# Kernel optimization log

Hardware: AMD Instinct MI355X
Metric: run time of the kernel (lower is better)

The kernel has to match this reference:

```python
import jax, jax.numpy as jnp
import numpy as np
from jax import lax

SEQ_SIZE = 4096
V = 4                               # vocab size
B = 256                             # batch
FILTER_SIZES = [4, 5, 6, 7, 8]
H = 10                              # lstm hidden
I = (len(FILTER_SIZES) + 1) * V     # lstm input size = 24


def setup_inputs() -> dict:
    key = jax.random.key(0)
    ks = jax.random.split(key, 9)
    inp = {"x": jax.random.normal(ks[0], (B, 1, V * SEQ_SIZE), dtype=jnp.float32)}
    for fs in FILTER_SIZES:
        # matches nn.init.constant_(conv.weight, 0.01)
        inp[f"w{fs}"] = jnp.full((1, 1, fs), 0.01, dtype=jnp.float32)
    s = 1.0 / float(np.sqrt(H))
    shapes = {"Wih": (4 * H, I), "Whh": (4 * H, H), "bih": (4 * H,), "bhh": (4 * H,)}
    k = 1
    for d in ("f", "r"):
        for nm, sh in shapes.items():
            inp[f"{nm}_{d}"] = jax.random.uniform(ks[k], sh, jnp.float32, -s, s)
            k += 1
    return inp


def _branch(x, w, fs):
    # x: (B,1,V*S); conv1d stride=V, VALID, no bias -> (B,1,L)
    conv = lax.conv_general_dilated(x, w, window_strides=(V,), padding="VALID",
                                    dimension_numbers=("NCH", "OIH", "NCH"))
    # winner_takes_all: (x + max_over_len)^2
    m = jnp.max(conv, axis=2, keepdims=True)
    v = ((conv + m) ** 2)[:, 0, :]                                  # (B,L)
    Bsz, L = v.shape
    # shape_convolutions2 == scatter-add of v[b,i] into out[b, V*i + j], j<fs
    idx = (V * jnp.arange(L)[:, None] + jnp.arange(fs)[None, :]).reshape(-1)
    contrib = jnp.broadcast_to(v[:, :, None], (Bsz, L, fs)).reshape(Bsz, -1)
    out = jnp.zeros((Bsz, V * SEQ_SIZE), v.dtype).at[:, idx].add(contrib)
    return out.reshape(Bsz, SEQ_SIZE, V)


def _lstm_dir(xs, Wih, Whh, bih, bhh, reverse):
    # xs: (S,B,I) -> hidden states (S,B,H), aligned with input positions
    Bsz = xs.shape[1]
    h0 = jnp.zeros((Bsz, H), xs.dtype)
    c0 = jnp.zeros((Bsz, H), xs.dtype)
    b = bih + bhh

    def step(carry, xt):
        h, c = carry
        g = xt @ Wih.T + h @ Whh.T + b          # (B,4H), torch gate order i,f,g,o
        i, f, gg, o = jnp.split(g, 4, axis=1)
        c = jax.nn.sigmoid(f) * c + jax.nn.sigmoid(i) * jnp.tanh(gg)
        h = jax.nn.sigmoid(o) * jnp.tanh(c)
        return (h, c), h

    _, hs = lax.scan(step, (h0, c0), xs, reverse=reverse)
    return hs


def _forward(x, ws, Wih_f, Whh_f, bih_f, bhh_f, Wih_r, Whh_r, bih_r, bhh_r):
    Bsz = x.shape[0]
    branches = [_branch(x, w, fs) for w, fs in zip(ws, FILTER_SIZES)]
    inp_r = x.reshape(Bsz, SEQ_SIZE, V)
    l_lstmin = jnp.concatenate(branches + [inp_r], axis=2)   # (B,S,24)
    xs = jnp.swapaxes(l_lstmin, 0, 1)                        # (S,B,24)
    hf = _lstm_dir(xs, Wih_f, Whh_f, bih_f, bhh_f, False)
    hr = _lstm_dir(xs, Wih_r, Whh_r, bih_r, bhh_r, True)
    h_sum = jnp.sum(hf, axis=2) + jnp.sum(hr, axis=2)        # (S,B)
    h_sum = h_sum.T                                          # (B,S)
    # l_in * repeated h_sum, reshaped and summed over vocab == inp_r * h_sum
    l_profile = jnp.sum(inp_r * h_sum[:, :, None], axis=2)   # (B,S)
    return jax.nn.sigmoid(jnp.sum(l_profile, axis=1, keepdims=True))  # (B,1)


def reference(x, w4, w5, w6, w7, w8, Wih_f, Whh_f, bih_f, bhh_f, Wih_r, Whh_r, bih_r, bhh_r):
    return _forward(x, [w4, w5, w6, w7, w8],
                    Wih_f, Whh_f, bih_f, bhh_f, Wih_r, Whh_r, bih_r, bhh_r)
```

## Files before the change

### kernel.cpp

```cpp
#include <hip/hip_runtime.h>

#define SEQ 4096
#define NBATCH 256

typedef float v2f __attribute__((ext_vector_type(2)));

__device__ __forceinline__ float sqf(float v) { return v * v; }
__device__ __forceinline__ float fexp2(float v) { return __builtin_amdgcn_exp2f(v); }
__device__ __forceinline__ float frcp(float v)  { return __builtin_amdgcn_rcpf(v); }

#define L2E 1.4426950408889634f

__device__ __forceinline__ unsigned fkey(float f) {
    const int b = __float_as_int(f);
    return (unsigned)(b ^ ((b >> 31) | 0x80000000));
}
__device__ __forceinline__ float fival(unsigned k) {
    const int b = (k & 0x80000000u) ? (int)(k ^ 0x80000000u) : (int)(~k);
    return __int_as_float(b);
}

__global__ void wprep_kernel(
    const float* __restrict__ Wih_f, const float* __restrict__ bih_f,
    const float* __restrict__ bhh_f,
    const float* __restrict__ Wih_r, const float* __restrict__ bih_r,
    const float* __restrict__ bhh_r,
    float* __restrict__ Wp, unsigned* __restrict__ MMu)
{
    const int t = threadIdx.x;
    for (int i = t; i < NBATCH * 5; i += 256) MMu[i] = 0u;
    if (t >= 80) return;
    const int d = t / 40, r = t % 40;
    const float* __restrict__ W  = (d ? Wih_r : Wih_f) + r * 24;
    const float* __restrict__ bi = d ? bih_r : bih_f;
    const float* __restrict__ bh = d ? bhh_r : bhh_f;
    const float sc = (r >= 20 && r < 30) ? (-2.f * L2E) : (-L2E);
    float o[13];
    o[0]  = W[0] + W[1] + W[2] + W[3];
    o[1]  = W[4] + W[5] + W[6] + W[7];
    o[2]  = W[4];
    o[3]  = W[8] + W[9] + W[10] + W[11];
    o[4]  = W[8] + W[9];
    o[5]  = W[12] + W[13] + W[14] + W[15];
    o[6]  = W[12] + W[13] + W[14];
    o[7]  = W[16] + W[17] + W[18] + W[19];
    o[8]  = W[20]; o[9] = W[21]; o[10] = W[22]; o[11] = W[23];
    o[12] = bi[r] + bh[r];
    float* __restrict__ out = Wp + (d * 40 + r) * 16;
#pragma unroll
    for (int k = 0; k < 13; ++k) out[k] = o[k] * sc;
    out[13] = 0.f; out[14] = 0.f; out[15] = 0.f;
}

__global__ __launch_bounds__(256) void max_kernel(
    const float* __restrict__ x,
    const float* __restrict__ w4p, const float* __restrict__ w5p,
    const float* __restrict__ w6p, const float* __restrict__ w7p,
    const float* __restrict__ w8p,
    unsigned* __restrict__ MMu)
{
    const int b    = blockIdx.x >> 2;
    const int quar = blockIdx.x & 3;
    const int tid  = threadIdx.x;
    const float* __restrict__ xr = x + (size_t)b * (4 * SEQ);

    float W4[4], W5[5], W6[6], W7[7], W8[8];
#pragma unroll
    for (int k = 0; k < 4; ++k) W4[k] = w4p[k];
#pragma unroll
    for (int k = 0; k < 5; ++k) W5[k] = w5p[k];
#pragma unroll
    for (int k = 0; k < 6; ++k) W6[k] = w6p[k];
#pragma unroll
    for (int k = 0; k < 7; ++k) W7[k] = w7p[k];
#pragma unroll
    for (int k = 0; k < 8; ++k) W8[k] = w8p[k];

    float m4 = -3.4e38f, m5 = -3.4e38f, m6 = -3.4e38f, m7 = -3.4e38f, m8 = -3.4e38f;
    for (int i = quar * (SEQ / 4) + tid; i < (quar + 1) * (SEQ / 4); i += 256) {
        const float4 t0 = *reinterpret_cast<const float4*>(xr + 4 * i);
        const float xa0 = t0.x, xa1 = t0.y, xa2 = t0.z, xa3 = t0.w;
        const float c4 = xa0 * W4[0] + xa1 * W4[1] + xa2 * W4[2] + xa3 * W4[3];
        m4 = fmaxf(m4, c4);
        if (i < SEQ - 1) {
            const float4 t1 = *reinterpret_cast<const float4*>(xr + 4 * i + 4);
            const float xa4 = t1.x, xa5 = t1.y, xa6 = t1.z, xa7 = t1.w;
            const float c5 = xa0*W5[0]+xa1*W5[1]+xa2*W5[2]+xa3*W5[3]+xa4*W5[4];
            const float c6 = xa0*W6[0]+xa1*W6[1]+xa2*W6[2]+xa3*W6[3]+xa4*W6[4]+xa5*W6[5];
            const float c7 = xa0*W7[0]+xa1*W7[1]+xa2*W7[2]+xa3*W7[3]+xa4*W7[4]+xa5*W7[5]+xa6*W7[6];
            const float c8 = xa0*W8[0]+xa1*W8[1]+xa2*W8[2]+xa3*W8[3]+xa4*W8[4]+xa5*W8[5]+xa6*W8[6]+xa7*W8[7];
            m5 = fmaxf(m5, c5); m6 = fmaxf(m6, c6);
            m7 = fmaxf(m7, c7); m8 = fmaxf(m8, c8);
        }
    }
#pragma unroll
    for (int off = 32; off; off >>= 1) {
        m4 = fmaxf(m4, __shfl_down(m4, off));
        m5 = fmaxf(m5, __shfl_down(m5, off));
        m6 = fmaxf(m6, __shfl_down(m6, off));
        m7 = fmaxf(m7, __shfl_down(m7, off));
        m8 = fmaxf(m8, __shfl_down(m8, off));
    }
    __shared__ float wr[4][5];
    if ((tid & 63) == 0) {
        const int w = tid >> 6;
        wr[w][0] = m4; wr[w][1] = m5; wr[w][2] = m6; wr[w][3] = m7; wr[w][4] = m8;
    }
    __syncthreads();
    if (tid < 5) {
        const float m = fmaxf(fmaxf(wr[0][tid], wr[1][tid]),
                              fmaxf(wr[2][tid], wr[3][tid]));
        atomicMax(&MMu[b * 5 + tid], fkey(m));
    }
}

__global__ __launch_bounds__(256) void scatter_kernel(
    const float* __restrict__ x,
    const float* __restrict__ w4p, const float* __restrict__ w5p,
    const float* __restrict__ w6p, const float* __restrict__ w7p,
    const float* __restrict__ w8p,
    const unsigned* __restrict__ MMu,
    float* __restrict__ lin)
{
    const int b    = blockIdx.x >> 2;
    const int quar = blockIdx.x & 3;
    const int tid  = threadIdx.x;
    const float* __restrict__ xr = x + (size_t)b * (4 * SEQ);

    float W4[4], W5[5], W6[6], W7[7], W8[8];
#pragma unroll
    for (int k = 0; k < 4; ++k) W4[k] = w4p[k];
#pragma unroll
    for (int k = 0; k < 5; ++k) W5[k] = w5p[k];
#pragma unroll
    for (int k = 0; k < 6; ++k) W6[k] = w6p[k];
#pragma unroll
    for (int k = 0; k < 7; ++k) W7[k] = w7p[k];
#pragma unroll
    for (int k = 0; k < 8; ++k) W8[k] = w8p[k];

    const float M4 = fival(MMu[b * 5 + 0]), M5 = fival(MMu[b * 5 + 1]),
                M6 = fival(MMu[b * 5 + 2]), M7 = fival(MMu[b * 5 + 3]),
                M8 = fival(MMu[b * 5 + 4]);

    for (int s = quar * (SEQ / 4) + tid; s < (quar + 1) * (SEQ / 4); s += 256) {
        float xw[12];
        if (s > 0) {
            const float4 t = *reinterpret_cast<const float4*>(xr + 4 * s - 4);
            xw[0] = t.x; xw[1] = t.y; xw[2] = t.z; xw[3] = t.w;
        } else { xw[0] = xw[1] = xw[2] = xw[3] = 0.f; }
        {
            const float4 t = *reinterpret_cast<const float4*>(xr + 4 * s);
            xw[4] = t.x; xw[5] = t.y; xw[6] = t.z; xw[7] = t.w;
        }
        if (s < SEQ - 1) {
            const float4 t = *reinterpret_cast<const float4*>(xr + 4 * s + 4);
            xw[8] = t.x; xw[9] = t.y; xw[10] = t.z; xw[11] = t.w;
        } else { xw[8] = xw[9] = xw[10] = xw[11] = 0.f; }

        float c4s = 0.f, c5s = 0.f, c6s = 0.f, c7s = 0.f, c8s = 0.f;
        float c5p = 0.f, c6p = 0.f, c7p = 0.f, c8p = 0.f;
#pragma unroll
        for (int t = 0; t < 4; ++t) c4s += xw[4 + t] * W4[t];
#pragma unroll
        for (int t = 0; t < 5; ++t) { c5s += xw[4 + t] * W5[t]; c5p += xw[t] * W5[t]; }
#pragma unroll
        for (int t = 0; t < 6; ++t) { c6s += xw[4 + t] * W6[t]; c6p += xw[t] * W6[t]; }
#pragma unroll
        for (int t = 0; t < 7; ++t) { c7s += xw[4 + t] * W7[t]; c7p += xw[t] * W7[t]; }
#pragma unroll
        for (int t = 0; t < 8; ++t) { c8s += xw[4 + t] * W8[t]; c8p += xw[t] * W8[t]; }

        const bool oks = (s < SEQ - 1);
        const bool okp = (s > 0);
        const float v4s = sqf(c4s + M4);
        const float v5s = oks ? sqf(c5s + M5) : 0.f;
        const float v6s = oks ? sqf(c6s + M6) : 0.f;
        const float v7s = oks ? sqf(c7s + M7) : 0.f;
        const float v8s = oks ? sqf(c8s + M8) : 0.f;
        const float v5p = okp ? sqf(c5p + M5) : 0.f;
        const float v6p = okp ? sqf(c6p + M6) : 0.f;
        const float v7p = okp ? sqf(c7p + M7) : 0.f;
        const float v8p = okp ? sqf(c8p + M8) : 0.f;

        const float xsum = (xw[4] + xw[5]) + (xw[6] + xw[7]);
        float4* op = reinterpret_cast<float4*>(lin + ((size_t)b * SEQ + s) * 16);
        op[0] = make_float4(v4s, v5s, v5p, v6s);
        op[1] = make_float4(v6p, v7s, v7p, v8s + v8p);
        op[2] = make_float4(xw[4], xw[5], xw[6], xw[7]);
        op[3] = make_float4(xsum, 0.f, 0.f, 0.f);
    }
}

__global__ __launch_bounds__(64) void lstm_kernel(
    const float* __restrict__ lin,
    const float* __restrict__ Wp,
    const float* __restrict__ Whh_f,
    const float* __restrict__ Whh_r,
    float* __restrict__ P)
{
    const int bg   = blockIdx.x & 63;
    const int d    = (blockIdx.x >> 6) & 1;
    const int q    = blockIdx.x >> 7;
    const int b0   = bg * 4;
    const int lane = threadIdx.x;

    const int segA = 2 * q, segB = 2 * q + 1;
    const int s0A = segA * 256 - 128;
    const int s0B = segB * 256 - 128;
    const int nChunks = 24, warmChunks = 8;

    __shared__ float gbufA[16 * 4 * 44];
    __shared__ float gbufB[16 * 4 * 44];
    __shared__ float xbufA[64];
    __shared__ float xbufB[64];
    __shared__ float hbA[64];
    __shared__ float hbB[64];

    const int c   = lane >> 4;
    const int jr  = lane & 15;
    const int jc  = (jr < 10) ? jr : 0;

    hbA[lane] = 0.f;
    hbB[lane] = 0.f;

    const float* __restrict__ Whh = d ? Whh_r : Whh_f;
    v2f wIF[10], wGO[10];
#pragma unroll
    for (int k = 0; k < 10; ++k) {
        wIF[k] = (v2f){Whh[jc * 10 + k]        * (-L2E),
                       Whh[(10 + jc) * 10 + k] * (-L2E)};
        wGO[k] = (v2f){Whh[(20 + jc) * 10 + k] * (-2.f * L2E),
                       Whh[(30 + jc) * 10 + k] * (-L2E)};
    }

    const float* __restrict__ Wd = Wp + d * 640;

    const int cc = lane & 3;
    const int r  = lane >> 2;
    const float* __restrict__ chbase = lin + (size_t)(b0 + cc) * SEQ * 16;

    auto rowp = [&](int s0, int cn) {
        int sp = s0 + cn * 16 + r;
        if (sp < 0) sp = 0;
        const int pos = d ? (SEQ - 1 - sp) : sp;
        return reinterpret_cast<const float4*>(chbase + (size_t)pos * 16);
    };

    float4 pA[4], pB[4];
    {
        const float4* a = rowp(s0A, 0);
        pA[0] = a[0]; pA[1] = a[1]; pA[2] = a[2]; pA[3] = a[3];
        const float4* bq = rowp(s0B, 0);
        pB[0] = bq[0]; pB[1] = bq[1]; pB[2] = bq[2]; pB[3] = bq[3];
    }

    float csA = 0.f, accSA = 0.f;
    float csB = 0.f, accSB = 0.f;

    auto step = [&](const float* gb, const float* xb, float* hb,
                    float& csv, float& aS, int i) {
        const float4 gp4 =
            *reinterpret_cast<const float4*>(&gb[(i * 4 + c) * 44 + jc * 4]);
        const float sx = xb[i * 4 + c];
        const float4 h03 = *reinterpret_cast<const float4*>(&hb[c * 16 + 0]);
        const float4 h47 = *reinterpret_cast<const float4*>(&hb[c * 16 + 4]);
        const float2 h89 = *reinterpret_cast<const float2*>(&hb[c * 16 + 8]);
        const float hj[10] = {h03.x, h03.y, h03.z, h03.w,
                              h47.x, h47.y, h47.z, h47.w, h89.x, h89.y};
        v2f eif0 = (v2f){gp4.x, gp4.y}, eif1 = (v2f){0.f, 0.f};
        v2f ego0 = (v2f){gp4.z, gp4.w}, ego1 = (v2f){0.f, 0.f};
#pragma unroll
        for (int k = 0; k < 10; k += 2) {
            const v2f h0 = (v2f){hj[k], hj[k]};
            const v2f h1 = (v2f){hj[k + 1], hj[k + 1]};
            eif0 += h0 * wIF[k]; eif1 += h1 * wIF[k + 1];
            ego0 += h0 * wGO[k]; ego1 += h1 * wGO[k + 1];
        }
        const v2f eif = eif0 + eif1, ego = ego0 + ego1;
        const float Ai = fexp2(eif.x);
        const float Fv = fexp2(eif.y);
        const float Bg = fexp2(fminf(ego.x, 80.f));
        const float Ov = fexp2(ego.y);
        const float sf = frcp(1.f + Fv);
        const float it = fmaf(Bg, 2.f * L2E, -2.f * L2E) *
                         frcp((1.f + Ai) * (1.f + Bg));
        csv = fmaf(sf, csv, it);
        const float Dv = fexp2(fminf(csv, 80.f));
        const float hv = (1.f - Dv) * frcp((1.f + Ov) * (1.f + Dv));
        hb[c * 16 + jr] = hv;
        aS = fmaf(sx, hv, aS);
    };

    for (int cn = 0; cn < nChunks; ++cn) {
        const float4 cA0 = pA[0], cA1 = pA[1], cA2 = pA[2], cA3 = pA[3];
        const float4 cB0 = pB[0], cB1 = pB[1], cB2 = pB[2], cB3 = pB[3];
        {
            const int nc = (cn + 1 < nChunks) ? cn + 1 : cn;
            const float4* a = rowp(s0A, nc);
            pA[0] = a[0]; pA[1] = a[1]; pA[2] = a[2]; pA[3] = a[3];
            const float4* bq = rowp(s0B, nc);
            pB[0] = bq[0]; pB[1] = bq[1]; pB[2] = bq[2]; pB[3] = bq[3];
        }
        xbufA[r * 4 + cc] = cA3.x;
        xbufB[r * 4 + cc] = cB3.x;
        v2f vab[12];
        vab[0]  = (v2f){cA0.x, cB0.x}; vab[1]  = (v2f){cA0.y, cB0.y};
        vab[2]  = (v2f){cA0.z, cB0.z}; vab[3]  = (v2f){cA0.w, cB0.w};
        vab[4]  = (v2f){cA1.x, cB1.x}; vab[5]  = (v2f){cA1.y, cB1.y};
        vab[6]  = (v2f){cA1.z, cB1.z}; vab[7]  = (v2f){cA1.w, cB1.w};
        vab[8]  = (v2f){cA2.x, cB2.x}; vab[9]  = (v2f){cA2.y, cB2.y};
        vab[10] = (v2f){cA2.z, cB2.z}; vab[11] = (v2f){cA2.w, cB2.w};
        const int wb = (r * 4 + cc) * 44;
#pragma unroll 2
        for (int j = 0; j < 10; ++j) {
            float oA[4], oB[4];
#pragma unroll
            for (int g = 0; g < 4; ++g) {
                const int rr = g * 10 + j;
                const float4 w0 = *reinterpret_cast<const float4*>(Wd + rr * 16 + 0);
                const float4 w1 = *reinterpret_cast<const float4*>(Wd + rr * 16 + 4);
                const float4 w2 = *reinterpret_cast<const float4*>(Wd + rr * 16 + 8);
                const float  bb = Wd[rr * 16 + 12];
                v2f a0 = (v2f){bb, bb}, a1 = (v2f){0.f, 0.f};
                v2f a2 = (v2f){0.f, 0.f}, a3 = (v2f){0.f, 0.f};
                a0 += vab[0]  * (v2f){w0.x, w0.x}; a1 += vab[1]  * (v2f){w0.y, w0.y};
                a2 += vab[2]  * (v2f){w0.z, w0.z}; a3 += vab[3]  * (v2f){w0.w, w0.w};
                a0 += vab[4]  * (v2f){w1.x, w1.x}; a1 += vab[5]  * (v2f){w1.y, w1.y};
                a2 += vab[6]  * (v2f){w1.z, w1.z}; a3 += vab[7]  * (v2f){w1.w, w1.w};
                a0 += vab[8]  * (v2f){w2.x, w2.x}; a1 += vab[9]  * (v2f){w2.y, w2.y};
                a2 += vab[10] * (v2f){w2.z, w2.z}; a3 += vab[11] * (v2f){w2.w, w2.w};
                const v2f s = (a0 + a1) + (a2 + a3);
                oA[g] = s.x; oB[g] = s.y;
            }
            *reinterpret_cast<float4*>(&gbufA[wb + j * 4]) =
                make_float4(oA[0], oA[1], oA[2], oA[3]);
            *reinterpret_cast<float4*>(&gbufB[wb + j * 4]) =
                make_float4(oB[0], oB[1], oB[2], oB[3]);
        }
        asm volatile("s_waitcnt lgkmcnt(0)" ::: "memory");
#pragma unroll 4
        for (int i = 0; i < 16; ++i) {
            step(gbufA, xbufA, hbA, csA, accSA, i);
            step(gbufB, xbufB, hbB, csB, accSB, i);
        }
        if (cn + 1 == warmChunks) {
            accSA = 0.f; accSB = 0.f;
            if (q == 0) {
                csA = 0.f;
                hbA[lane] = 0.f;
            }
        }
    }

    float vA = (jr < 10) ? accSA : 0.f;
    float vB = (jr < 10) ? accSB : 0.f;
#pragma unroll
    for (int off = 1; off <= 8; off <<= 1) {
        vA += __shfl_down(vA, off);
        vB += __shfl_down(vB, off);
    }
    if (jr == 0) {
        P[segA * 512 + d * 256 + b0 + c] = vA;
        P[segB * 512 + d * 256 + b0 + c] = vB;
    }
}

__global__ __launch_bounds__(256) void final_kernel(const float* __restrict__ P,
                                                    float* __restrict__ out)
{
    const int b = threadIdx.x;
    float v = 0.f;
#pragma unroll
    for (int seg = 0; seg < 16; ++seg)
        v += P[seg * 512 + b] + P[seg * 512 + 256 + b];
    out[b] = frcp(1.f + fexp2(-v * L2E));
}

extern "C" void kernel_launch(void* const* d_in, const int* in_sizes, int n_in,
                              void* d_out, int out_size, void* d_ws, size_t ws_size,
                              hipStream_t stream)
{
    const float* x     = (const float*)d_in[0];
    const float* w4    = (const float*)d_in[1];
    const float* w5    = (const float*)d_in[2];
    const float* w6    = (const float*)d_in[3];
    const float* w7    = (const float*)d_in[4];
    const float* w8    = (const float*)d_in[5];
    const float* Wih_f = (const float*)d_in[6];
    const float* Whh_f = (const float*)d_in[7];
    const float* bih_f = (const float*)d_in[8];
    const float* bhh_f = (const float*)d_in[9];
    const float* Wih_r = (const float*)d_in[10];
    const float* Whh_r = (const float*)d_in[11];
    const float* bih_r = (const float*)d_in[12];
    const float* bhh_r = (const float*)d_in[13];

    float*    lin = (float*)d_ws;
    float*    P   = lin + (size_t)NBATCH * SEQ * 16;
    unsigned* MMu = (unsigned*)(P + 8192);
    float*    Wpp = (float*)(MMu + 1280);

    wprep_kernel<<<1, 256, 0, stream>>>(Wih_f, bih_f, bhh_f,
                                        Wih_r, bih_r, bhh_r, Wpp, MMu);
    max_kernel<<<4 * NBATCH, 256, 0, stream>>>(x, w4, w5, w6, w7, w8, MMu);
    scatter_kernel<<<4 * NBATCH, 256, 0, stream>>>(x, w4, w5, w6, w7, w8, MMu, lin);
    lstm_kernel<<<1024, 64, 0, stream>>>(lin, Wpp, Whh_f, Whh_r, P);
    final_kernel<<<1, NBATCH, 0, stream>>>(P, (float*)d_out);
}
```

Baseline: 277.1 us.

## Process one LSTM segment per block and double the grid size

After: 269.6 us. 1.03x faster.

```diff
diff --git a/kernel.cpp b/kernel.cpp
--- a/kernel.cpp
+++ b/kernel.cpp
@@ -192,7 +192,7 @@
     }
 }
 
-__global__ __launch_bounds__(64) void lstm_kernel(
+__global__ __launch_bounds__(64, 2) void lstm_kernel(
     const float* __restrict__ lin,
     const float* __restrict__ Wp,
     const float* __restrict__ Whh_f,
@@ -205,24 +205,18 @@
     const int b0   = bg * 4;
     const int lane = threadIdx.x;
 
-    const int segA = 2 * q, segB = 2 * q + 1;
-    const int s0A = segA * 256 - 128;
-    const int s0B = segB * 256 - 128;
+    const int s0 = q * 256 - 128;
     const int nChunks = 24, warmChunks = 8;
 
-    __shared__ float gbufA[16 * 4 * 44];
-    __shared__ float gbufB[16 * 4 * 44];
-    __shared__ float xbufA[64];
-    __shared__ float xbufB[64];
-    __shared__ float hbA[64];
-    __shared__ float hbB[64];
+    __shared__ float gbuf[16 * 4 * 44];
+    __shared__ float xbuf[64];
+    __shared__ float hb[64];
 
     const int c   = lane >> 4;
     const int jr  = lane & 15;
     const int jc  = (jr < 10) ? jr : 0;
 
-    hbA[lane] = 0.f;
-    hbB[lane] = 0.f;
+    hb[lane] = 0.f;
 
     const float* __restrict__ Whh = d ? Whh_r : Whh_f;
     v2f wIF[10], wGO[10];
@@ -240,29 +234,25 @@
     const int r  = lane >> 2;
     const float* __restrict__ chbase = lin + (size_t)(b0 + cc) * SEQ * 16;
 
-    auto rowp = [&](int s0, int cn) {
+    auto rowp = [&](int cn) {
         int sp = s0 + cn * 16 + r;
         if (sp < 0) sp = 0;
         const int pos = d ? (SEQ - 1 - sp) : sp;
         return reinterpret_cast<const float4*>(chbase + (size_t)pos * 16);
     };
 
-    float4 pA[4], pB[4];
+    float4 pA[4];
     {
-        const float4* a = rowp(s0A, 0);
+        const float4* a = rowp(0);
         pA[0] = a[0]; pA[1] = a[1]; pA[2] = a[2]; pA[3] = a[3];
-        const float4* bq = rowp(s0B, 0);
-        pB[0] = bq[0]; pB[1] = bq[1]; pB[2] = bq[2]; pB[3] = bq[3];
-    }
-
-    float csA = 0.f, accSA = 0.f;
-    float csB = 0.f, accSB = 0.f;
-
-    auto step = [&](const float* gb, const float* xb, float* hb,
-                    float& csv, float& aS, int i) {
+    }
+
+    float cs = 0.f, accS = 0.f;
+
+    auto step = [&](int i) {
         const float4 gp4 =
-            *reinterpret_cast<const float4*>(&gb[(i * 4 + c) * 44 + jc * 4]);
-        const float sx = xb[i * 4 + c];
+            *reinterpret_cast<const float4*>(&gbuf[(i * 4 + c) * 44 + jc * 4]);
+        const float sx = xbuf[i * 4 + c];
         const float4 h03 = *reinterpret_cast<const float4*>(&hb[c * 16 + 0]);
         const float4 h47 = *reinterpret_cast<const float4*>(&hb[c * 16 + 4]);
         const float2 h89 = *reinterpret_cast<const float2*>(&hb[c * 16 + 8]);
@@ -285,85 +275,63 @@
         const float sf = frcp(1.f + Fv);
         const float it = fmaf(Bg, 2.f * L2E, -2.f * L2E) *
                          frcp((1.f + Ai) * (1.f + Bg));
-        csv = fmaf(sf, csv, it);
-        const float Dv = fexp2(fminf(csv, 80.f));
+        cs = fmaf(sf, cs, it);
+        const float Dv = fexp2(fminf(cs, 80.f));
         const float hv = (1.f - Dv) * frcp((1.f + Ov) * (1.f + Dv));
         hb[c * 16 + jr] = hv;
-        aS = fmaf(sx, hv, aS);
+        accS = fmaf(sx, hv, accS);
     };
 
     for (int cn = 0; cn < nChunks; ++cn) {
         const float4 cA0 = pA[0], cA1 = pA[1], cA2 = pA[2], cA3 = pA[3];
-        const float4 cB0 = pB[0], cB1 = pB[1], cB2 = pB[2], cB3 = pB[3];
         {
             const int nc = (cn + 1 < nChunks) ? cn + 1 : cn;
-            const float4* a = rowp(s0A, nc);
+            const float4* a = rowp(nc);
             pA[0] = a[0]; pA[1] = a[1]; pA[2] = a[2]; pA[3] = a[3];
-            const float4* bq = rowp(s0B, nc);
-            pB[0] = bq[0]; pB[1] = bq[1]; pB[2] = bq[2]; pB[3] = bq[3];
-        }
-        xbufA[r * 4 + cc] = cA3.x;
-        xbufB[r * 4 + cc] = cB3.x;
-        v2f vab[12];
-        vab[0]  = (v2f){cA0.x, cB0.x}; vab[1]  = (v2f){cA0.y, cB0.y};
-        vab[2]  = (v2f){cA0.z, cB0.z}; vab[3]  = (v2f){cA0.w, cB0.w};
-        vab[4]  = (v2f){cA1.x, cB1.x}; vab[5]  = (v2f){cA1.y, cB1.y};
-        vab[6]  = (v2f){cA1.z, cB1.z}; vab[7]  = (v2f){cA1.w, cB1.w};
-        vab[8]  = (v2f){cA2.x, cB2.x}; vab[9]  = (v2f){cA2.y, cB2.y};
-        vab[10] = (v2f){cA2.z, cB2.z}; vab[11] = (v2f){cA2.w, cB2.w};
+        }
+        xbuf[r * 4 + cc] = cA3.x;
+        float vv[12];
+        vv[0] = cA0.x; vv[1] = cA0.y; vv[2]  = cA0.z; vv[3]  = cA0.w;
+        vv[4] = cA1.x; vv[5] = cA1.y; vv[6]  = cA1.z; vv[7]  = cA1.w;
+        vv[8] = cA2.x; vv[9] = cA2.y; vv[10] = cA2.z; vv[11] = cA2.w;
         const int wb = (r * 4 + cc) * 44;
 #pragma unroll 2
         for (int j = 0; j < 10; ++j) {
-            float oA[4], oB[4];
-#pragma unroll
-            for (int g = 0; g < 4; ++g) {
-                const int rr = g * 10 + j;
-                const float4 w0 = *reinterpret_cast<const float4*>(Wd + rr * 16 + 0);
-                const float4 w1 = *reinterpret_cast<const float4*>(Wd + rr * 16 + 4);
-                const float4 w2 = *reinterpret_cast<const float4*>(Wd + rr * 16 + 8);
-                const float  bb = Wd[rr * 16 + 12];
-                v2f a0 = (v2f){bb, bb}, a1 = (v2f){0.f, 0.f};
-                v2f a2 = (v2f){0.f, 0.f}, a3 = (v2f){0.f, 0.f};
-                a0 += vab[0]  * (v2f){w0.x, w0.x}; a1 += vab[1]  * (v2f){w0.y, w0.y};
-                a2 += vab[2]  * (v2f){w0.z, w0.z}; a3 += vab[3]  * (v2f){w0.w, w0.w};
-                a0 += vab[4]  * (v2f){w1.x, w1.x}; a1 += vab[5]  * (v2f){w1.y, w1.y};
-                a2 += vab[6]  * (v2f){w1.z, w1.z}; a3 += vab[7]  * (v2f){w1.w, w1.w};
-                a0 += vab[8]  * (v2f){w2.x, w2.x}; a1 += vab[9]  * (v2f){w2.y, w2.y};
-                a2 += vab[10] * (v2f){w2.z, w2.z}; a3 += vab[11] * (v2f){w2.w, w2.w};
-                const v2f s = (a0 + a1) + (a2 + a3);
-                oA[g] = s.x; oB[g] = s.y;
+            const float* __restrict__ R0 = Wd + j * 16;
+            const float* __restrict__ R1 = Wd + (10 + j) * 16;
+            const float* __restrict__ R2 = Wd + (20 + j) * 16;
+            const float* __restrict__ R3 = Wd + (30 + j) * 16;
+            v2f a01 = (v2f){R0[12], R1[12]}, b01 = (v2f){0.f, 0.f};
+            v2f a23 = (v2f){R2[12], R3[12]}, b23 = (v2f){0.f, 0.f};
+#pragma unroll
+            for (int k = 0; k < 12; k += 2) {
+                const v2f vk0 = (v2f){vv[k], vv[k]};
+                const v2f vk1 = (v2f){vv[k + 1], vv[k + 1]};
+                a01 += vk0 * (v2f){R0[k], R1[k]};
+                b01 += vk1 * (v2f){R0[k + 1], R1[k + 1]};
+                a23 += vk0 * (v2f){R2[k], R3[k]};
+                b23 += vk1 * (v2f){R2[k + 1], R3[k + 1]};
             }
-            *reinterpret_cast<float4*>(&gbufA[wb + j * 4]) =
-                make_float4(oA[0], oA[1], oA[2], oA[3]);
-            *reinterpret_cast<float4*>(&gbufB[wb + j * 4]) =
-                make_float4(oB[0], oB[1], oB[2], oB[3]);
+            const v2f s01 = a01 + b01, s23 = a23 + b23;
+            *reinterpret_cast<float4*>(&gbuf[wb + j * 4]) =
+                make_float4(s01.x, s01.y, s23.x, s23.y);
         }
         asm volatile("s_waitcnt lgkmcnt(0)" ::: "memory");
 #pragma unroll 4
-        for (int i = 0; i < 16; ++i) {
-            step(gbufA, xbufA, hbA, csA, accSA, i);
-            step(gbufB, xbufB, hbB, csB, accSB, i);
-        }
+        for (int i = 0; i < 16; ++i) step(i);
         if (cn + 1 == warmChunks) {
-            accSA = 0.f; accSB = 0.f;
+            accS = 0.f;
             if (q == 0) {
-                csA = 0.f;
-                hbA[lane] = 0.f;
+                cs = 0.f;
+                hb[lane] = 0.f;
             }
         }
     }
 
-    float vA = (jr < 10) ? accSA : 0.f;
-    float vB = (jr < 10) ? accSB : 0.f;
-#pragma unroll
-    for (int off = 1; off <= 8; off <<= 1) {
-        vA += __shfl_down(vA, off);
-        vB += __shfl_down(vB, off);
-    }
-    if (jr == 0) {
-        P[segA * 512 + d * 256 + b0 + c] = vA;
-        P[segB * 512 + d * 256 + b0 + c] = vB;
-    }
+    float vA = (jr < 10) ? accS : 0.f;
+#pragma unroll
+    for (int off = 1; off <= 8; off <<= 1) vA += __shfl_down(vA, off);
+    if (jr == 0) P[q * 512 + d * 256 + b0 + c] = vA;
 }
 
 __global__ __launch_bounds__(256) void final_kernel(const float* __restrict__ P,
@@ -405,6 +373,6 @@
                                         Wih_r, bih_r, bhh_r, Wpp, MMu);
     max_kernel<<<4 * NBATCH, 256, 0, stream>>>(x, w4, w5, w6, w7, w8, MMu);
     scatter_kernel<<<4 * NBATCH, 256, 0, stream>>>(x, w4, w5, w6, w7, w8, MMu, lin);
-    lstm_kernel<<<1024, 64, 0, stream>>>(lin, Wpp, Whh_f, Whh_r, P);
+    lstm_kernel<<<2048, 64, 0, stream>>>(lin, Wpp, Whh_f, Whh_r, P);
     final_kernel<<<1, NBATCH, 0, stream>>>(P, (float*)d_out);
 }
```
